# Performance work log

Hardware: AMD Instinct MI355X
Metric: run time of the kernel (lower is better)

The kernel has to match this reference:

```python
import jax, jax.numpy as jnp
import numpy as np

N = 10000        # nodes
E = 320000       # edges
IN = 256         # input_dim
D = 64           # output_dim per head
H = 4            # num_heads
ED = 32          # edge_dim
T = 8            # num_etypes
SLOPE = 0.2      # leaky relu negative slope


def setup_inputs() -> dict:
    key = jax.random.key(0)
    ks = jax.random.split(key, 12)
    s = 0.05
    feat = jax.random.normal(ks[0], (N, IN), jnp.float32)
    edge_weight = jax.random.uniform(ks[1], (E,), jnp.float32)
    row = jax.random.randint(ks[2], (E,), 0, N, jnp.int32)
    col = jax.random.randint(ks[3], (E,), 0, N, jnp.int32)
    etype_idxs = jax.random.randint(ks[4], (E,), 0, T, jnp.int32)
    W = jax.random.normal(ks[5], (IN, D * H), jnp.float32) * s
    edge_emb_table = jax.random.normal(ks[6], (T, ED), jnp.float32) * s
    W_r = jax.random.normal(ks[7], (T, ED, ED * H), jnp.float32) * s
    a_l = jax.random.normal(ks[8], (H, D), jnp.float32) * s
    a_r = jax.random.normal(ks[9], (H, D), jnp.float32) * s
    a_e = jax.random.normal(ks[10], (H, ED), jnp.float32) * s
    W_res = jax.random.normal(ks[11], (IN, D * H), jnp.float32) * s
    b_res = jnp.zeros((D * H,), jnp.float32)
    return dict(feat=feat, edge_weight=edge_weight, row=row, col=col,
                etype_idxs=etype_idxs, W=W, edge_emb_table=edge_emb_table,
                W_r=W_r, a_l=a_l, a_r=a_r, a_e=a_e, W_res=W_res, b_res=b_res)


def reference(feat, edge_weight, row, col, etype_idxs, W, edge_emb_table,
              W_r, a_l, a_r, a_e, W_res, b_res):
    # node projection: [N, H, D]
    emb = jnp.nan_to_num(feat @ W).reshape(N, H, D)
    # typed linear on edge-type embeddings: only T distinct outputs, gather per edge
    type_out = jnp.einsum('ti,tio->to', edge_emb_table, W_r).reshape(T, H, ED)
    edge_e = type_out[etype_idxs]                      # [E, H, ED]
    # attention logits
    hl = jnp.einsum('nhd,hd->nh', emb, a_l)            # [N, H]
    hr = jnp.einsum('nhd,hd->nh', emb, a_r)            # [N, H]
    he = jnp.einsum('ehd,hd->eh', edge_e, a_e)         # [E, H]
    att = jax.nn.sigmoid(jax.nn.leaky_relu(hl[row] + hr[col] + he, SLOPE))
    att = att * edge_weight[:, None]                   # [E, H]
    # u_mul_e + sum scatter: src=row, dst=col
    msg = emb[row] * att[:, :, None]                   # [E, H, D]
    agg = jax.ops.segment_sum(msg, col, num_segments=N)  # [N, H, D]
    # original permutes to [N, D, H] before flattening
    out = jnp.transpose(agg, (0, 2, 1)).reshape(N, D * H)
    out = out + feat @ W_res + b_res                   # residual
    return jax.nn.elu(out)
```

## Files before the change

### kernel.cpp

```cpp
#include <hip/hip_runtime.h>
#include <hip/hip_bf16.h>
#include <math.h>

#define N_NODES 10000
#define MPAD 10112
#define N_EDGES 320000
#define IN_DIM 256
#define NH 4
#define EDIM 32
#define NT 8
#define SLOPE 0.2f
#define CAP 96

#define WTW (512 * 256)
#define GB (MPAD / 64)
#define EBT 512
#define EB ((N_EDGES + EBT - 1) / EBT)

typedef __attribute__((ext_vector_type(8))) short short8b;
typedef __attribute__((ext_vector_type(4))) float f32x4;

__device__ __forceinline__ float bf2f(ushort u) {
  return __uint_as_float(((unsigned)u) << 16);
}
__device__ __forceinline__ ushort f2bf(float f) {
  __hip_bfloat16 h = __float2bfloat16(f);
  return *(ushort*)&h;
}
__device__ __forceinline__ unsigned pk2(float a, float b) {
  return (unsigned)f2bf(a) | ((unsigned)f2bf(b) << 16);
}

__global__ void prep_kernel(const float* __restrict__ W,
                            const float* __restrict__ W_res,
                            const float* __restrict__ table,
                            const float* __restrict__ W_r,
                            const float* __restrict__ a_e,
                            ushort* __restrict__ Wtb,
                            float* __restrict__ he_type,
                            int* __restrict__ cnt) {
  int i = blockIdx.x * 256 + threadIdx.x;
  if (i < WTW) {
    int c = i >> 8, k = i & 255;
    float v = (c < 256) ? W[k * 256 + ((c & 3) * 64 + (c >> 2))]
                        : W_res[k * 256 + (c - 256)];
    Wtb[c * 256 + k] = f2bf(v);
  } else if (i < WTW + 1024) {
    int t2 = i - WTW;
    int t = t2 >> 7, h = (t2 >> 5) & 3, d = t2 & 31;
    float acc = 0.f;
    for (int q = 0; q < EDIM; ++q)
      acc += table[t * EDIM + q] * W_r[(t * EDIM + q) * (EDIM * NH) + h * EDIM + d];
    acc *= a_e[h * EDIM + d];
#pragma unroll
    for (int o = 16; o; o >>= 1) acc += __shfl_xor(acc, o, 32);
    if (d == 0) he_type[t * NH + h] = acc;
  } else {
    int z = i - WTW - 1024;
    if (z <= N_NODES) cnt[z] = 0;
  }
}

__global__ __launch_bounds__(512) void gemm_bucket_kernel(
    const float* __restrict__ feat, const ushort* __restrict__ Wtb,
    const float* __restrict__ b_res,
    const float* __restrict__ a_l, const float* __restrict__ a_r,
    ushort* __restrict__ emb_t, ushort* __restrict__ resb,
    float* __restrict__ hl, float* __restrict__ hr,
    const int* __restrict__ row, const int* __restrict__ colv,
    const int* __restrict__ et, const float* __restrict__ ew,
    int* cnt, uint2* __restrict__ slots) {
  __shared__ ushort As[64 * 256];
  const int tid = threadIdx.x;

  if (blockIdx.x >= GB) {
    int e = (blockIdx.x - GB) * EBT + tid;
    if (e < N_EDGES) {
      int r = row[e], c = colv[e], t = et[e];
      float w = ew[e];
      uint2 slot;
      slot.x = ((unsigned)t << 16) | (unsigned)r;
      slot.y = __float_as_uint(w);
      int s = atomicAdd(&cnt[c], 1);
      if (s < CAP) slots[(size_t)c * CAP + s] = slot;
    }
    return;
  }

  const int rowbase = blockIdx.x * 64;

#pragma unroll
  for (int i = 0; i < 4; ++i) {
    int c = tid + i * 512;
    int rowl = c >> 5, slot = c & 31;
    int gr = rowbase + rowl;
    uint4 pk = make_uint4(0, 0, 0, 0);
    if (gr < N_NODES) {
      float4 x = *(const float4*)&feat[(size_t)gr * 256 + slot * 8];
      float4 y = *(const float4*)&feat[(size_t)gr * 256 + slot * 8 + 4];
      pk.x = pk2(x.x, x.y); pk.y = pk2(x.z, x.w);
      pk.z = pk2(y.x, y.y); pk.w = pk2(y.z, y.w);
    }
    int idx = rowl * 256 + (((slot * 16) ^ ((rowl & 7) << 4)) >> 1);
    *(uint4*)&As[idx] = pk;
  }
  __syncthreads();

  const int wave = tid >> 6, lane = tid & 63;
  const int col0 = wave * 64;
  const int lr = lane & 15;
  const int lkq = lane >> 4;
  f32x4 acc[4][4] = {};
  const ushort* Bb = Wtb + (size_t)(col0 + lr) * 256 + lkq * 8;

#pragma unroll
  for (int ks = 0; ks < 8; ++ks) {
    short8b a[4], b[4];
#pragma unroll
    for (int m = 0; m < 4; ++m) {
      int rowl = m * 16 + lr;
      int kb = ks * 64 + lkq * 16;
      int idx = rowl * 256 + ((kb ^ ((rowl & 7) << 4)) >> 1);
      a[m] = *(const short8b*)&As[idx];
    }
#pragma unroll
    for (int n = 0; n < 4; ++n)
      b[n] = *(const short8b*)(Bb + (size_t)(n * 16) * 256 + ks * 32);
#pragma unroll
    for (int n = 0; n < 4; ++n)
#pragma unroll
      for (int m = 0; m < 4; ++m)
        acc[n][m] = __builtin_amdgcn_mfma_f32_16x16x32_bf16(b[n], a[m], acc[n][m], 0, 0, 0);
  }

  float pl[4][4] = {{0.f}}, pr[4][4] = {{0.f}};
  if (col0 < 256) {
#pragma unroll
    for (int m = 0; m < 4; ++m) {
      int r = rowbase + m * 16 + lr;
      if (r < N_NODES) {
#pragma unroll
        for (int n = 0; n < 4; ++n) {
          int d = (col0 >> 2) + n * 4 + lkq;
          ushort4 pk4;
          pk4.x = f2bf(acc[n][m][0]); pk4.y = f2bf(acc[n][m][1]);
          pk4.z = f2bf(acc[n][m][2]); pk4.w = f2bf(acc[n][m][3]);
          *(ushort4*)&emb_t[((size_t)r * 64 + d) * 4] = pk4;
        }
      }
    }
#pragma unroll
    for (int n = 0; n < 4; ++n) {
      int d = (col0 >> 2) + n * 4 + lkq;
#pragma unroll
      for (int h = 0; h < 4; ++h) {
        float alv = a_l[h * 64 + d];
        float arv = a_r[h * 64 + d];
#pragma unroll
        for (int m = 0; m < 4; ++m) {
          pl[m][h] = fmaf(acc[n][m][h], alv, pl[m][h]);
          pr[m][h] = fmaf(acc[n][m][h], arv, pr[m][h]);
        }
      }
    }
#pragma unroll
    for (int m = 0; m < 4; ++m)
#pragma unroll
      for (int h = 0; h < 4; ++h) {
        pl[m][h] += __shfl_xor(pl[m][h], 16);
        pl[m][h] += __shfl_xor(pl[m][h], 32);
        pr[m][h] += __shfl_xor(pr[m][h], 16);
        pr[m][h] += __shfl_xor(pr[m][h], 32);
      }
  } else {
#pragma unroll
    for (int m = 0; m < 4; ++m) {
      int r = rowbase + m * 16 + lr;
      if (r < N_NODES) {
#pragma unroll
        for (int n = 0; n < 4; ++n) {
          int c = (col0 - 256) + n * 16 + lkq * 4;
          float4 br = *(const float4*)&b_res[c];
          ushort4 pk4;
          pk4.x = f2bf(acc[n][m][0] + br.x); pk4.y = f2bf(acc[n][m][1] + br.y);
          pk4.z = f2bf(acc[n][m][2] + br.z); pk4.w = f2bf(acc[n][m][3] + br.w);
          *(ushort4*)&resb[(size_t)r * 256 + c] = pk4;
        }
      }
    }
  }

  float* PL = (float*)As;
  float* PR = PL + 1024;
  __syncthreads();
  if (col0 < 256 && lkq == 0) {
#pragma unroll
    for (int m = 0; m < 4; ++m)
#pragma unroll
      for (int h = 0; h < 4; ++h) {
        PL[(wave * 64 + m * 16 + lr) * 4 + h] = pl[m][h];
        PR[(wave * 64 + m * 16 + lr) * 4 + h] = pr[m][h];
      }
  }
  __syncthreads();
  if (tid < 128) {
    int rl = tid >> 1, sel = tid & 1;
    const float* P = sel ? PR : PL;
    float4 v;
    v.x = P[rl * 4 + 0] + P[256 + rl * 4 + 0] + P[512 + rl * 4 + 0] + P[768 + rl * 4 + 0];
    v.y = P[rl * 4 + 1] + P[256 + rl * 4 + 1] + P[512 + rl * 4 + 1] + P[768 + rl * 4 + 1];
    v.z = P[rl * 4 + 2] + P[256 + rl * 4 + 2] + P[512 + rl * 4 + 2] + P[768 + rl * 4 + 2];
    v.w = P[rl * 4 + 3] + P[256 + rl * 4 + 3] + P[512 + rl * 4 + 3] + P[768 + rl * 4 + 3];
    int gr = rowbase + rl;
    if (gr < N_NODES) *(float4*)&(sel ? hr : hl)[gr * 4] = v;
  }
}

__global__ __launch_bounds__(256) void agg_kernel(
    const int* __restrict__ cnt, const uint2* __restrict__ slots,
    const float* __restrict__ hl, const float* __restrict__ hr,
    const float* __restrict__ he_type,
    const ushort* __restrict__ emb_t, const ushort* __restrict__ resb,
    float* __restrict__ out) {
  __shared__ uint4 meta[4 * CAP];
  const int wv = threadIdx.x >> 6;
  const int lane = threadIdx.x & 63;
  const int nu = __builtin_amdgcn_readfirstlane(blockIdx.x * 4 + wv);
  const int cn = min(cnt[nu], CAP);

  {
    float4 R = *(const float4*)&hr[nu * 4];
    for (int j = lane; j < cn; j += 64) {
      uint2 s = slots[(size_t)nu * CAP + j];
      int src = s.x & 0xffff, t = s.x >> 16;
      float w = __uint_as_float(s.y);
      float4 L = *(const float4*)&hl[src * 4];
      float4 He = *(const float4*)&he_type[t * 4];
      float x[4] = {L.x + R.x + He.x, L.y + R.y + He.y,
                    L.z + R.z + He.z, L.w + R.w + He.w};
      float a[4];
#pragma unroll
      for (int h = 0; h < 4; ++h) {
        float v = x[h];
        v = v >= 0.f ? v : SLOPE * v;
        a[h] = w / (1.f + __expf(-v));
      }
      uint4 m;
      m.x = pk2(a[0], a[1]);
      m.y = pk2(a[2], a[3]);
      m.z = (unsigned)src;
      m.w = 0;
      meta[wv * CAP + j] = m;
    }
  }
  __syncthreads();

  float acc0 = 0.f, acc1 = 0.f, acc2 = 0.f, acc3 = 0.f;
  const uint4* mb = &meta[wv * CAP];

#define AGG_FMA(V, WA, WB)                                      \
  acc0 = fmaf(bf2f((V).x), __uint_as_float((WA) << 16), acc0);  \
  acc1 = fmaf(bf2f((V).y), __uint_as_float((WA) & 0xffff0000u), acc1); \
  acc2 = fmaf(bf2f((V).z), __uint_as_float((WB) << 16), acc2);  \
  acc3 = fmaf(bf2f((V).w), __uint_as_float((WB) & 0xffff0000u), acc3);

  const int j4 = cn & ~3;
#pragma unroll 2
  for (int j = 0; j < j4; j += 4) {
    uint4 m0 = mb[j], m1 = mb[j + 1], m2 = mb[j + 2], m3 = mb[j + 3];
    ushort4 v0 = *(const ushort4*)&emb_t[((size_t)m0.z * 64 + lane) * 4];
    ushort4 v1 = *(const ushort4*)&emb_t[((size_t)m1.z * 64 + lane) * 4];
    ushort4 v2 = *(const ushort4*)&emb_t[((size_t)m2.z * 64 + lane) * 4];
    ushort4 v3 = *(const ushort4*)&emb_t[((size_t)m3.z * 64 + lane) * 4];
    AGG_FMA(v0, m0.x, m0.y)
    AGG_FMA(v1, m1.x, m1.y)
    AGG_FMA(v2, m2.x, m2.y)
    AGG_FMA(v3, m3.x, m3.y)
  }
  for (int j = j4; j < cn; ++j) {
    uint4 m0 = mb[j];
    ushort4 v0 = *(const ushort4*)&emb_t[((size_t)m0.z * 64 + lane) * 4];
    AGG_FMA(v0, m0.x, m0.y)
  }
#undef AGG_FMA

  ushort4 r4 = *(const ushort4*)&resb[((size_t)nu * 64 + lane) * 4];
  float v0 = acc0 + bf2f(r4.x), v1 = acc1 + bf2f(r4.y);
  float v2 = acc2 + bf2f(r4.z), v3 = acc3 + bf2f(r4.w);
  float4 o;
  o.x = v0 > 0.f ? v0 : expm1f(v0);
  o.y = v1 > 0.f ? v1 : expm1f(v1);
  o.z = v2 > 0.f ? v2 : expm1f(v2);
  o.w = v3 > 0.f ? v3 : expm1f(v3);
  *(float4*)&out[((size_t)nu * 64 + lane) * 4] = o;
}

extern "C" void kernel_launch(void* const* d_in, const int* in_sizes, int n_in,
                              void* d_out, int out_size, void* d_ws, size_t ws_size,
                              hipStream_t stream) {
  const float* feat = (const float*)d_in[0];
  const float* ew = (const float*)d_in[1];
  const int* row = (const int*)d_in[2];
  const int* col = (const int*)d_in[3];
  const int* etype = (const int*)d_in[4];
  const float* W = (const float*)d_in[5];
  const float* table = (const float*)d_in[6];
  const float* W_r = (const float*)d_in[7];
  const float* a_l = (const float*)d_in[8];
  const float* a_r = (const float*)d_in[9];
  const float* a_e = (const float*)d_in[10];
  const float* W_res = (const float*)d_in[11];
  const float* b_res = (const float*)d_in[12];
  float* out = (float*)d_out;

  char* w = (char*)d_ws;
  auto alloc = [&](size_t bytes) {
    char* pp = w;
    w += (bytes + 255) & ~(size_t)255;
    return pp;
  };
  ushort* Wtb = (ushort*)alloc((size_t)512 * 256 * 2);
  ushort* emb_t = (ushort*)alloc((size_t)N_NODES * 256 * 2);
  ushort* resb = (ushort*)alloc((size_t)N_NODES * 256 * 2);
  uint2* slots = (uint2*)alloc((size_t)N_NODES * CAP * 8);
  float* hl = (float*)alloc((size_t)N_NODES * NH * 4);
  float* hr = (float*)alloc((size_t)N_NODES * NH * 4);
  float* he_type = (float*)alloc(NT * NH * 4);
  int* cnt = (int*)alloc((size_t)(N_NODES + 1) * 4);

  const int PREP_BLOCKS = WTW / 256 + 4 + (N_NODES + 256) / 256;
  prep_kernel<<<PREP_BLOCKS, 256, 0, stream>>>(W, W_res, table, W_r, a_e,
                                               Wtb, he_type, cnt);
  gemm_bucket_kernel<<<GB + EB, 512, 0, stream>>>(
      feat, Wtb, b_res, a_l, a_r, emb_t, resb, hl, hr,
      row, col, etype, ew, cnt, slots);
  agg_kernel<<<N_NODES / 4, 256, 0, stream>>>(cnt, slots, hl, hr, he_type,
                                              emb_t, resb, out);
}
```

Baseline: 52.38 us.

## Tile weight transpose through LDS, fuse attention-logit reduction per row, relax agg barrier

The prep kernel now transposes W and W_res in 64x64 tiles staged through shared memory, with vectorized coalesced loads and packed 16-byte bf16 stores. Previously it ran 131k threads, each doing a strided scalar load. The GEMM epilogue computes the hl/hr partial dot products per row group and writes them straight to LDS, so it holds fewer live registers. A block-wide barrier in the aggregation kernel becomes a wave barrier, which is valid only if each wave reads just its own metadata slice. The weight transpose is off the main path, so the overall effect is probably small.

```diff
diff --git a/kernel.cpp b/kernel.cpp
--- a/kernel.cpp
+++ b/kernel.cpp
@@ -12,11 +12,15 @@
 #define SLOPE 0.2f
 #define CAP 96
 
-#define WTW (512 * 256)
 #define GB (MPAD / 64)
 #define EBT 512
 #define EB ((N_EDGES + EBT - 1) / EBT)
 
+#define PREP_WT_BLOCKS 32
+#define PREP_HE_BLOCKS 4
+#define PREP_Z_BLOCKS 40
+#define PREP_BLOCKS (PREP_WT_BLOCKS + PREP_HE_BLOCKS + PREP_Z_BLOCKS)
+
 typedef __attribute__((ext_vector_type(8))) short short8b;
 typedef __attribute__((ext_vector_type(4))) float f32x4;
 
@@ -31,22 +35,47 @@
   return (unsigned)f2bf(a) | ((unsigned)f2bf(b) << 16);
 }
 
-__global__ void prep_kernel(const float* __restrict__ W,
-                            const float* __restrict__ W_res,
-                            const float* __restrict__ table,
-                            const float* __restrict__ W_r,
-                            const float* __restrict__ a_e,
-                            ushort* __restrict__ Wtb,
-                            float* __restrict__ he_type,
-                            int* __restrict__ cnt) {
-  int i = blockIdx.x * 256 + threadIdx.x;
-  if (i < WTW) {
-    int c = i >> 8, k = i & 255;
-    float v = (c < 256) ? W[k * 256 + ((c & 3) * 64 + (c >> 2))]
-                        : W_res[k * 256 + (c - 256)];
-    Wtb[c * 256 + k] = f2bf(v);
-  } else if (i < WTW + 1024) {
-    int t2 = i - WTW;
+__global__ __launch_bounds__(256) void prep_kernel(
+    const float* __restrict__ W, const float* __restrict__ W_res,
+    const float* __restrict__ table, const float* __restrict__ W_r,
+    const float* __restrict__ a_e, ushort* __restrict__ Wtb,
+    float* __restrict__ he_type, int* __restrict__ cnt) {
+  const int b = blockIdx.x;
+  const int tid = threadIdx.x;
+  if (b < PREP_WT_BLOCKS) {
+    __shared__ float Ls[64][68];
+    const bool isres = b >= 16;
+    const float* src = isres ? W_res : W;
+    const int t = b & 15;
+    const int k0 = (t >> 2) * 64, c0 = (t & 3) * 64;
+    {
+      int r = tid >> 2, cc = (tid & 3) * 16;
+      const float* sp = &src[(size_t)(k0 + r) * 256 + c0 + cc];
+      float4 v0 = ((const float4*)sp)[0];
+      float4 v1 = ((const float4*)sp)[1];
+      float4 v2 = ((const float4*)sp)[2];
+      float4 v3 = ((const float4*)sp)[3];
+      *(float4*)&Ls[r][cc + 0] = v0;
+      *(float4*)&Ls[r][cc + 4] = v1;
+      *(float4*)&Ls[r][cc + 8] = v2;
+      *(float4*)&Ls[r][cc + 12] = v3;
+    }
+    __syncthreads();
+    {
+      int cloc = tid >> 2, kc = (tid & 3) * 16;
+      int csrc = c0 + cloc;
+      int cdst = isres ? (256 + csrc) : (((csrc & 63) << 2) | (csrc >> 6));
+      unsigned u[8];
+#pragma unroll
+      for (int q = 0; q < 8; ++q)
+        u[q] = pk2(Ls[kc + 2 * q][cloc], Ls[kc + 2 * q + 1][cloc]);
+      uint4 w0 = make_uint4(u[0], u[1], u[2], u[3]);
+      uint4 w1 = make_uint4(u[4], u[5], u[6], u[7]);
+      *(uint4*)&Wtb[(size_t)cdst * 256 + k0 + kc] = w0;
+      *(uint4*)&Wtb[(size_t)cdst * 256 + k0 + kc + 8] = w1;
+    }
+  } else if (b < PREP_WT_BLOCKS + PREP_HE_BLOCKS) {
+    int t2 = (b - PREP_WT_BLOCKS) * 256 + tid;
     int t = t2 >> 7, h = (t2 >> 5) & 3, d = t2 & 31;
     float acc = 0.f;
     for (int q = 0; q < EDIM; ++q)
@@ -56,7 +85,7 @@
     for (int o = 16; o; o >>= 1) acc += __shfl_xor(acc, o, 32);
     if (d == 0) he_type[t * NH + h] = acc;
   } else {
-    int z = i - WTW - 1024;
+    int z = (b - PREP_WT_BLOCKS - PREP_HE_BLOCKS) * 256 + tid;
     if (z <= N_NODES) cnt[z] = 0;
   }
 }
@@ -133,11 +162,14 @@
         acc[n][m] = __builtin_amdgcn_mfma_f32_16x16x32_bf16(b[n], a[m], acc[n][m], 0, 0, 0);
   }
 
-  float pl[4][4] = {{0.f}}, pr[4][4] = {{0.f}};
+  __syncthreads();
+  float* PL = (float*)As;
+  float* PR = PL + 1024;
+
   if (col0 < 256) {
 #pragma unroll
     for (int m = 0; m < 4; ++m) {
-      int r = rowbase + m * 16 + lr;
+      const int r = rowbase + m * 16 + lr;
       if (r < N_NODES) {
 #pragma unroll
         for (int n = 0; n < 4; ++n) {
@@ -148,34 +180,35 @@
           *(ushort4*)&emb_t[((size_t)r * 64 + d) * 4] = pk4;
         }
       }
-    }
-#pragma unroll
-    for (int n = 0; n < 4; ++n) {
-      int d = (col0 >> 2) + n * 4 + lkq;
+      float pl[4] = {0.f, 0.f, 0.f, 0.f}, pr[4] = {0.f, 0.f, 0.f, 0.f};
+#pragma unroll
+      for (int n = 0; n < 4; ++n) {
+        int d = (col0 >> 2) + n * 4 + lkq;
+#pragma unroll
+        for (int h = 0; h < 4; ++h) {
+          pl[h] = fmaf(acc[n][m][h], a_l[h * 64 + d], pl[h]);
+          pr[h] = fmaf(acc[n][m][h], a_r[h * 64 + d], pr[h]);
+        }
+      }
 #pragma unroll
       for (int h = 0; h < 4; ++h) {
-        float alv = a_l[h * 64 + d];
-        float arv = a_r[h * 64 + d];
-#pragma unroll
-        for (int m = 0; m < 4; ++m) {
-          pl[m][h] = fmaf(acc[n][m][h], alv, pl[m][h]);
-          pr[m][h] = fmaf(acc[n][m][h], arv, pr[m][h]);
+        pl[h] += __shfl_xor(pl[h], 16);
+        pl[h] += __shfl_xor(pl[h], 32);
+        pr[h] += __shfl_xor(pr[h], 16);
+        pr[h] += __shfl_xor(pr[h], 32);
+      }
+      if (lkq == 0) {
+#pragma unroll
+        for (int h = 0; h < 4; ++h) {
+          PL[(wave * 64 + m * 16 + lr) * 4 + h] = pl[h];
+          PR[(wave * 64 + m * 16 + lr) * 4 + h] = pr[h];
         }
       }
     }
-#pragma unroll
-    for (int m = 0; m < 4; ++m)
-#pragma unroll
-      for (int h = 0; h < 4; ++h) {
-        pl[m][h] += __shfl_xor(pl[m][h], 16);
-        pl[m][h] += __shfl_xor(pl[m][h], 32);
-        pr[m][h] += __shfl_xor(pr[m][h], 16);
-        pr[m][h] += __shfl_xor(pr[m][h], 32);
-      }
   } else {
 #pragma unroll
     for (int m = 0; m < 4; ++m) {
-      int r = rowbase + m * 16 + lr;
+      const int r = rowbase + m * 16 + lr;
       if (r < N_NODES) {
 #pragma unroll
         for (int n = 0; n < 4; ++n) {
@@ -190,18 +223,6 @@
     }
   }
 
-  float* PL = (float*)As;
-  float* PR = PL + 1024;
-  __syncthreads();
-  if (col0 < 256 && lkq == 0) {
-#pragma unroll
-    for (int m = 0; m < 4; ++m)
-#pragma unroll
-      for (int h = 0; h < 4; ++h) {
-        PL[(wave * 64 + m * 16 + lr) * 4 + h] = pl[m][h];
-        PR[(wave * 64 + m * 16 + lr) * 4 + h] = pr[m][h];
-      }
-  }
   __syncthreads();
   if (tid < 128) {
     int rl = tid >> 1, sel = tid & 1;
@@ -253,7 +274,7 @@
       meta[wv * CAP + j] = m;
     }
   }
-  __syncthreads();
+  __builtin_amdgcn_wave_barrier();
 
   float acc0 = 0.f, acc1 = 0.f, acc2 = 0.f, acc3 = 0.f;
   const uint4* mb = &meta[wv * CAP];
@@ -328,7 +349,6 @@
   float* he_type = (float*)alloc(NT * NH * 4);
   int* cnt = (int*)alloc((size_t)(N_NODES + 1) * 4);
 
-  const int PREP_BLOCKS = WTW / 256 + 4 + (N_NODES + 256) / 256;
   prep_kernel<<<PREP_BLOCKS, 256, 0, stream>>>(W, W_res, table, W_r, a_e,
                                                Wtb, he_type, cnt);
   gemm_bucket_kernel<<<GB + EB, 512, 0, stream>>>(
```

Measured after the change: 51.83 us. No clear change (-1.0%).
